# Performance work log

Hardware: AMD Instinct MI355X
Metric: run time of the kernel (lower is better)

The kernel has to match this reference:

```python
import jax, jax.numpy as jnp
import numpy as np

N_NODES = 50000
N_EDGES = 800000
NODE = 128
EDGE = 16
H = 96
OUT = 64
L = 3
BN_EPS = 1e-5


def setup_inputs() -> dict:
    key = jax.random.key(0)
    ks = iter(jax.random.split(key, 48))
    def rn(shape, s=0.05):
        return jax.random.normal(next(ks), shape, dtype=jnp.float32) * s
    inp = {
        "x": jax.random.normal(next(ks), (N_NODES, NODE), dtype=jnp.float32),
        "edge_index": jax.random.randint(next(ks), (2, N_EDGES), 0, N_NODES, dtype=jnp.int32),
        "edge_attr": jax.random.normal(next(ks), (N_EDGES, EDGE), dtype=jnp.float32),
        # GCNConv (layer 0)
        "gcn_lin_w": rn((NODE, H)), "gcn_lin_b": rn((H,)),
        "gcn_root": rn((1, H)),
        "gcn_bw1": rn((EDGE, H)), "gcn_bb1": rn((H,)),
        "gcn_bw2": rn((H, H)), "gcn_bb2": rn((H,)),
        # GINConv layers 1..L-1 (stacked)
        "gin_bw1": rn((L - 1, EDGE, H)), "gin_bb1": rn((L - 1, H)),
        "gin_bw2": rn((L - 1, H, H)), "gin_bb2": rn((L - 1, H)),
        "gin_mw1": rn((L - 1, H, H)), "gin_mb1": rn((L - 1, H)),
        "gin_mw2": rn((L - 1, H, H)), "gin_mb2": rn((L - 1, H)),
        "gin_eps": jnp.zeros((L - 1,), jnp.float32),
        # BatchNorm (eval mode, running stats)
        "bn_gamma": jnp.ones((L, H), jnp.float32),
        "bn_beta": jnp.zeros((L, H), jnp.float32),
        "bn_mean": rn((L, H)),
        "bn_var": jnp.ones((L, H), jnp.float32) + jax.random.uniform(next(ks), (L, H), dtype=jnp.float32) * 0.1,
        # head
        "fc1_w": rn((L * H, H)), "fc1_b": rn((H,)),
        "fc2_w": rn((H, OUT)), "fc2_b": rn((OUT,)),
    }
    return inp


def _bn(x, gamma, beta, mean, var):
    return (x - mean) * jax.lax.rsqrt(var + BN_EPS) * gamma + beta


def reference(x, edge_index, edge_attr,
              gcn_lin_w, gcn_lin_b, gcn_root, gcn_bw1, gcn_bb1, gcn_bw2, gcn_bb2,
              gin_bw1, gin_bb1, gin_bw2, gin_bb2, gin_mw1, gin_mb1, gin_mw2, gin_mb2, gin_eps,
              bn_gamma, bn_beta, bn_mean, bn_var,
              fc1_w, fc1_b, fc2_w, fc2_b):
    n = x.shape[0]
    row, col = edge_index[0], edge_index[1]  # source, target

    # ---- Layer 0: GCNConv with edge attributes ----
    h = x @ gcn_lin_w + gcn_lin_b                                    # [N,H]
    ee = jax.nn.relu(edge_attr @ gcn_bw1 + gcn_bb1) @ gcn_bw2 + gcn_bb2  # [E,H]
    deg = jax.ops.segment_sum(jnp.ones_like(row, dtype=h.dtype), row, num_segments=n) + 1.0
    dinv = jax.lax.rsqrt(deg)                                        # deg >= 1, no inf
    norm = dinv[row] * dinv[col]                                     # [E]
    msg = norm[:, None] * jax.nn.relu(h[row] + ee)                   # [E,H]
    agg = jax.ops.segment_sum(msg, col, num_segments=n)              # [N,H]
    h = agg + jax.nn.relu(h + gcn_root) / deg[:, None]
    h = _bn(jax.nn.relu(h), bn_gamma[0], bn_beta[0], bn_mean[0], bn_var[0])
    feats = [h]

    # ---- Layers 1..L-1: GINConv with edge attributes ----
    for i in range(L - 1):
        ee = jax.nn.relu(edge_attr @ gin_bw1[i] + gin_bb1[i]) @ gin_bw2[i] + gin_bb2[i]  # [E,H]
        agg = jax.ops.segment_sum(jax.nn.relu(h[row] + ee), col, num_segments=n)          # [N,H]
        z = (1.0 + gin_eps[i]) * h + agg
        z = jax.nn.relu(z @ gin_mw1[i] + gin_mb1[i]) @ gin_mw2[i] + gin_mb2[i]
        h = _bn(jax.nn.relu(z), bn_gamma[i + 1], bn_beta[i + 1], bn_mean[i + 1], bn_var[i + 1])
        feats.append(h)

    cat = jnp.concatenate(feats, axis=-1)                            # [N, L*H]
    y = jax.nn.relu(cat @ fc1_w + fc1_b)                             # dropout is eval-mode identity
    return y @ fc2_w + fc2_b                                         # [N, OUT]
```

## Files before the change

### kernel.cpp

```cpp
#include <hip/hip_runtime.h>
#include <hip/hip_bf16.h>


#define HH 96
#define EDGEF 16
#define CAT (3 * HH)

typedef __attribute__((ext_vector_type(8))) short bf16x8;
typedef __attribute__((ext_vector_type(4))) float f32x4;
typedef __attribute__((ext_vector_type(4))) unsigned short ubf16x4;
typedef __attribute__((ext_vector_type(2))) unsigned uint2v;

typedef union { bf16x8 v; unsigned u[4]; } bfpack8;
typedef union { ubf16x4 v; unsigned u[2]; } bfpack4;

__device__ __forceinline__ unsigned short f2bf(float f) {
    unsigned u = __float_as_uint(f);
    u += 0x7fffu + ((u >> 16) & 1u);
    return (unsigned short)(u >> 16);
}
__device__ __forceinline__ float bf2f(unsigned short s) {
    return __uint_as_float(((unsigned)s) << 16);
}
__device__ __forceinline__ unsigned pkbf2(float lo, float hi) {
    __hip_bfloat162 b = __float22bfloat162_rn(make_float2(lo, hi));
    union { __hip_bfloat162 b2; unsigned u; } cv; cv.b2 = b; return cv.u;
}

template <int K, int F, int AMODE, int EPI>
__global__ __launch_bounds__(256) void node_gemm(
    const void* __restrict__ Aptr, int lda,
    const float* __restrict__ agg,
    const float* __restrict__ eps_arr, int li,
    const float* __restrict__ W, const float* __restrict__ bias,
    void* __restrict__ Cptr, int ldc,
    unsigned short* __restrict__ bf_copy,
    const float* __restrict__ gamma, const float* __restrict__ beta,
    const float* __restrict__ mean, const float* __restrict__ var,
    int M)
{
    constexpr int SW = ((K * 2) % 128 == 0) ? 7 : 3;
    constexpr int NFT = F / 16;
    __shared__ __align__(16) short s_wt[F * K];

    const int tid = threadIdx.x;
    const int lane = tid & 63;
    const int w = tid >> 6;
    const int lr = lane & 15;
    const int lg = lane >> 4;

    for (int idx = tid; idx < F * K; idx += 256) {
        int f = idx / K, k = idx - f * K;
        s_wt[idx ^ ((f & SW) << 3)] = (short)f2bf(W[k * F + f]);
    }
    __syncthreads();

    const int R0 = blockIdx.x * 64 + 16 * w;
    const int Ra = min(R0 + lr, M - 1);

    float e1 = 0.f;
    if (AMODE == 2) e1 = 1.f + eps_arr[li];

    f32x4 acc[NFT];
#pragma unroll
    for (int ft = 0; ft < NFT; ++ft) {
        float b = bias[16 * ft + lr];
        acc[ft][0] = b; acc[ft][1] = b; acc[ft][2] = b; acc[ft][3] = b;
    }

#pragma unroll
    for (int kt = 0; kt < K / 32; ++kt) {
        bf16x8 ae;
        if (AMODE == 0) {
            const float* ap = (const float*)Aptr + (size_t)Ra * lda + 32 * kt + 8 * lg;
            f32x4 a0 = *(const f32x4*)ap;
            f32x4 a1 = *(const f32x4*)(ap + 4);
            bfpack8 p;
            p.u[0] = pkbf2(a0[0], a0[1]); p.u[1] = pkbf2(a0[2], a0[3]);
            p.u[2] = pkbf2(a1[0], a1[1]); p.u[3] = pkbf2(a1[2], a1[3]);
            ae = p.v;
        } else if (AMODE == 1) {
            ae = *(const bf16x8*)((const unsigned short*)Aptr + (size_t)Ra * lda + 32 * kt + 8 * lg);
        } else {
            const unsigned short* hp = (const unsigned short*)Aptr + (size_t)Ra * lda + 32 * kt + 8 * lg;
            bf16x8 h8 = *(const bf16x8*)hp;
            const float* gp = agg + (size_t)Ra * HH + 32 * kt + 8 * lg;
            f32x4 g0 = *(const f32x4*)gp;
            f32x4 g1 = *(const f32x4*)(gp + 4);
            float t0 = fmaf(e1, bf2f((unsigned short)h8[0]), g0[0]);
            float t1 = fmaf(e1, bf2f((unsigned short)h8[1]), g0[1]);
            float t2 = fmaf(e1, bf2f((unsigned short)h8[2]), g0[2]);
            float t3 = fmaf(e1, bf2f((unsigned short)h8[3]), g0[3]);
            float t4 = fmaf(e1, bf2f((unsigned short)h8[4]), g1[0]);
            float t5 = fmaf(e1, bf2f((unsigned short)h8[5]), g1[1]);
            float t6 = fmaf(e1, bf2f((unsigned short)h8[6]), g1[2]);
            float t7 = fmaf(e1, bf2f((unsigned short)h8[7]), g1[3]);
            bfpack8 p;
            p.u[0] = pkbf2(t0, t1); p.u[1] = pkbf2(t2, t3);
            p.u[2] = pkbf2(t4, t5); p.u[3] = pkbf2(t6, t7);
            ae = p.v;
        }
#pragma unroll
        for (int ft = 0; ft < NFT; ++ft) {
            bf16x8 bw = *(const bf16x8*)&s_wt[((lr + 16 * ft) * K + 32 * kt + 8 * lg) ^ ((lr & SW) << 3)];
            acc[ft] = __builtin_amdgcn_mfma_f32_16x16x32_bf16(ae, bw, acc[ft], 0, 0, 0);
        }
    }

    float scale[NFT], shiftv[NFT];
    if (EPI == 2) {
#pragma unroll
        for (int ft = 0; ft < NFT; ++ft) {
            int col = 16 * ft + lr;
            float s = gamma[col] * rsqrtf(var[col] + 1e-5f);
            scale[ft] = s;
            shiftv[ft] = beta[col] - mean[col] * s;
        }
    }
#pragma unroll
    for (int reg = 0; reg < 4; ++reg) {
        int r = R0 + 4 * lg + reg;
        if (r < M) {
#pragma unroll
            for (int ft = 0; ft < NFT; ++ft) {
                int col = 16 * ft + lr;
                float v = acc[ft][reg];
                if (EPI == 0) {
                    ((float*)Cptr)[(size_t)r * ldc + col] = v;
                } else if (EPI == 1) {
                    ((unsigned short*)Cptr)[(size_t)r * ldc + col] = f2bf(fmaxf(v, 0.f));
                } else if (EPI == 2) {
                    float z = fmaxf(v, 0.f) * scale[ft] + shiftv[ft];
                    unsigned short zb = f2bf(z);
                    ((unsigned short*)Cptr)[(size_t)r * ldc + col] = zb;
                    bf_copy[(size_t)r * F + col] = zb;
                } else {
                    ((float*)Cptr)[(size_t)r * ldc + col] = v;
                    bf_copy[(size_t)r * F + col] = f2bf(v);
                }
            }
        }
    }
}

__global__ void init_kernel(float* __restrict__ deg, int* __restrict__ cnt, int N)
{
    int i = blockIdx.x * blockDim.x + threadIdx.x;
    if (i < N) { deg[i] = 1.f; cnt[i] = 0; }
}

__global__ void count_kernel(const int* __restrict__ row, const int* __restrict__ col,
                             float* __restrict__ deg, int* __restrict__ cnt, int E)
{
    int e = blockIdx.x * blockDim.x + threadIdx.x;
    if (e < E) {
        atomicAdd(&deg[row[e]], 1.f);
        atomicAdd(&cnt[col[e]], 1);
    }
}

__global__ void scan1_kernel(const int* __restrict__ cnt, int* __restrict__ start,
                             int* __restrict__ bsum, int N)
{
    __shared__ int s[256];
    int tid = threadIdx.x;
    int i = blockIdx.x * 256 + tid;
    int v = (i < N) ? cnt[i] : 0;
    s[tid] = v;
    __syncthreads();
#pragma unroll
    for (int off = 1; off < 256; off <<= 1) {
        int t = (tid >= off) ? s[tid - off] : 0;
        __syncthreads();
        s[tid] += t;
        __syncthreads();
    }
    if (i < N) start[i] = s[tid] - v;
    if (tid == 255) bsum[blockIdx.x] = s[255];
}

__global__ void scan2_kernel(int* __restrict__ bsum, int nb)
{
    __shared__ int s[256];
    int tid = threadIdx.x;
    int v = (tid < nb) ? bsum[tid] : 0;
    s[tid] = v;
    __syncthreads();
#pragma unroll
    for (int off = 1; off < 256; off <<= 1) {
        int t = (tid >= off) ? s[tid - off] : 0;
        __syncthreads();
        s[tid] += t;
        __syncthreads();
    }
    if (tid < nb) bsum[tid] = s[tid] - v;
}

__global__ void scan3_kernel(int* __restrict__ start, const int* __restrict__ bsum,
                             int* __restrict__ cursor,
                             const float* __restrict__ deg, float* __restrict__ dinv,
                             int N, int E)
{
    int i = blockIdx.x * blockDim.x + threadIdx.x;
    if (i < N) {
        int f = start[i] + bsum[i >> 8];
        start[i] = f;
        cursor[i] = f;
        dinv[i] = rsqrtf(deg[i]);
    } else if (i == N) {
        start[N] = E;
    }
}

__global__ void scatter_ea_kernel(const int* __restrict__ row, const int* __restrict__ col,
                                  int* __restrict__ cursor,
                                  const float* __restrict__ ea,
                                  int* __restrict__ row_sorted,
                                  unsigned short* __restrict__ eas, int E)
{
    int e = blockIdx.x * blockDim.x + threadIdx.x;
    if (e >= E) return;
    int c = col[e];
    int p = atomicAdd(&cursor[c], 1);
    row_sorted[p] = row[e];
    const float* src = ea + (size_t)e * EDGEF;
    f32x4 v0 = *(const f32x4*)(src);
    f32x4 v1 = *(const f32x4*)(src + 4);
    f32x4 v2 = *(const f32x4*)(src + 8);
    f32x4 v3 = *(const f32x4*)(src + 12);
    bfpack8 o0, o1;
    o0.u[0] = pkbf2(v0[0], v0[1]); o0.u[1] = pkbf2(v0[2], v0[3]);
    o0.u[2] = pkbf2(v1[0], v1[1]); o0.u[3] = pkbf2(v1[2], v1[3]);
    o1.u[0] = pkbf2(v2[0], v2[1]); o1.u[1] = pkbf2(v2[2], v2[3]);
    o1.u[2] = pkbf2(v3[0], v3[1]); o1.u[3] = pkbf2(v3[2], v3[3]);
    *(bf16x8*)(eas + (size_t)p * EDGEF) = o0.v;
    *(bf16x8*)(eas + (size_t)p * EDGEF + 8) = o1.v;
}

template <bool GCN>
__global__ __launch_bounds__(256, 4) void edge_kernel(
    const unsigned short* __restrict__ ea_sorted,
    const int* __restrict__ row_sorted,
    const int* __restrict__ seg_start,
    const float* __restrict__ bw1, const float* __restrict__ bb1,
    const float* __restrict__ bw2, const float* __restrict__ bb2,
    const unsigned short* __restrict__ hbf,
    const float* __restrict__ dinv,
    float* __restrict__ agg,
    int N)
{
    __shared__ __align__(16) short s_bw2T[96][104];
    __shared__ __align__(16) short s_bw1T[96][16];
    __shared__ __align__(16) short s_t[4][16][104];
    __shared__ float s_bias[192];

    const int tid = threadIdx.x;
    const int lane = tid & 63;
    const int w = tid >> 6;
    const int lr = lane & 15;
    const int lg = lane >> 4;

    for (int idx = tid; idx < HH * HH; idx += 256) {
        int k = idx / HH, f = idx - k * HH;
        s_bw2T[f][k] = (short)f2bf(bw2[idx]);
    }
    for (int idx = tid; idx < EDGEF * HH; idx += 256) {
        int k = idx / HH, f = idx - k * HH;
        s_bw1T[f][k] = (short)f2bf(bw1[idx]);
    }
    if (tid < HH) { s_bias[tid] = bb1[tid]; s_bias[HH + tid] = bb2[tid]; }
    __syncthreads();

    bf16x8 bwf[6];
#pragma unroll
    for (int ft = 0; ft < 6; ++ft) {
        bf16x8 z;
#pragma unroll
        for (int j = 0; j < 8; ++j) z[j] = 0;
        if (lg < 2) z = *(const bf16x8*)&s_bw1T[lr + 16 * ft][8 * lg];
        bwf[ft] = z;
    }

    const int nwaves = gridDim.x * 4;

    for (int c = blockIdx.x * 4 + w; c < N; c += nwaves) {
        const int s0 = seg_start[c];
        const int s1 = seg_start[c + 1];
        const float dinv_c = GCN ? dinv[c] : 1.f;

        f32x4 acc[6];
#pragma unroll
        for (int ft = 0; ft < 6; ++ft) { acc[ft][0]=0.f; acc[ft][1]=0.f; acc[ft][2]=0.f; acc[ft][3]=0.f; }

        for (int b = s0; b < s1; b += 16) {
            const int epos = b + lr;
            const bool vld = (epos < s1);
            const int epc = vld ? epos : s0;
            const int r = row_sorted[epc];

            const unsigned short* hrow = hbf + (size_t)r * HH + 24 * lg;
            bf16x8 h0 = *(const bf16x8*)(hrow);
            bf16x8 h1 = *(const bf16x8*)(hrow + 8);
            bf16x8 h2 = *(const bf16x8*)(hrow + 16);

            const float msk = vld ? (GCN ? dinv[r] * dinv_c : 1.f) : 0.f;

            bf16x8 ae = *(const bf16x8*)(ea_sorted + (size_t)epc * EDGEF + 8 * (lg & 1));

#pragma unroll
            for (int ft = 0; ft < 6; ++ft) {
                f32x4 ci = *(const f32x4*)&s_bias[16 * ft + 4 * lg];
                f32x4 t4 = __builtin_amdgcn_mfma_f32_16x16x32_bf16(bwf[ft], ae, ci, 0, 0, 0);
                float v0 = fmaxf(t4[0], 0.f);
                float v1 = fmaxf(t4[1], 0.f);
                float v2 = fmaxf(t4[2], 0.f);
                float v3 = fmaxf(t4[3], 0.f);
                uint2v uu;
                uu[0] = pkbf2(v0, v1);
                uu[1] = pkbf2(v2, v3);
                *(uint2v*)&s_t[w][lr][16 * ft + 4 * lg] = uu;
            }
            __builtin_amdgcn_wave_barrier();

            bf16x8 bt[3];
#pragma unroll
            for (int kt = 0; kt < 3; ++kt)
                bt[kt] = *(const bf16x8*)&s_t[w][lr][8 * lg + 32 * kt];
            __builtin_amdgcn_wave_barrier();

            *(bf16x8*)&s_t[w][lr][24 * lg]      = h0;
            *(bf16x8*)&s_t[w][lr][24 * lg + 8]  = h1;
            *(bf16x8*)&s_t[w][lr][24 * lg + 16] = h2;
            __builtin_amdgcn_wave_barrier();

#pragma unroll
            for (int ft = 0; ft < 6; ++ft) {
                const int fb = 16 * ft + 4 * lg;
                f32x4 ee = *(const f32x4*)&s_bias[HH + fb];
#pragma unroll
                for (int kt = 0; kt < 3; ++kt) {
                    bf16x8 aw = *(const bf16x8*)&s_bw2T[lr + 16 * ft][8 * lg + 32 * kt];
                    ee = __builtin_amdgcn_mfma_f32_16x16x32_bf16(aw, bt[kt], ee, 0, 0, 0);
                }
                ubf16x4 hv = *(const ubf16x4*)&s_t[w][lr][fb];
#pragma unroll
                for (int reg = 0; reg < 4; ++reg) {
                    float m = fmaxf(bf2f(hv[reg]) + ee[reg], 0.f);
                    acc[ft][reg] = fmaf(m, msk, acc[ft][reg]);
                }
            }
        }

#pragma unroll
        for (int ft = 0; ft < 6; ++ft) {
#pragma unroll
            for (int reg = 0; reg < 4; ++reg) {
                float v = acc[ft][reg];
                v += __shfl_xor(v, 1);
                v += __shfl_xor(v, 2);
                v += __shfl_xor(v, 4);
                v += __shfl_xor(v, 8);
                acc[ft][reg] = v;
            }
        }
        if (lr == 0) {
#pragma unroll
            for (int ft = 0; ft < 6; ++ft)
                *(f32x4*)&agg[(size_t)c * HH + 16 * ft + 4 * lg] = acc[ft];
        }
    }
}

__global__ void gcn_epilogue_kernel(
    const float* __restrict__ agg, const float* __restrict__ hbuf,
    const float* __restrict__ root, const float* __restrict__ deg,
    const float* __restrict__ gamma, const float* __restrict__ beta,
    const float* __restrict__ mean, const float* __restrict__ var,
    unsigned short* __restrict__ featsbf, unsigned short* __restrict__ hb, int N)
{
    int idx = blockIdx.x * blockDim.x + threadIdx.x;
    if (idx >= N * (HH / 4)) return;
    int n = idx / (HH / 4), q = idx - n * (HH / 4);
    int f0 = 4 * q;
    f32x4 a  = *(const f32x4*)&agg[(size_t)n * HH + f0];
    f32x4 h  = *(const f32x4*)&hbuf[(size_t)n * HH + f0];
    f32x4 rt = *(const f32x4*)&root[f0];
    f32x4 gm = *(const f32x4*)&gamma[f0];
    f32x4 bt = *(const f32x4*)&beta[f0];
    f32x4 mn = *(const f32x4*)&mean[f0];
    f32x4 vr = *(const f32x4*)&var[f0];
    float di = 1.f / deg[n];
    float vv[4];
#pragma unroll
    for (int j = 0; j < 4; ++j) {
        float self = fmaxf(h[j] + rt[j], 0.f) * di;
        float v = fmaxf(a[j] + self, 0.f);
        vv[j] = (v - mn[j]) * rsqrtf(vr[j] + 1e-5f) * gm[j] + bt[j];
    }
    bfpack4 o;
    o.u[0] = pkbf2(vv[0], vv[1]);
    o.u[1] = pkbf2(vv[2], vv[3]);
    *(ubf16x4*)&featsbf[(size_t)n * CAT + f0] = o.v;
    *(ubf16x4*)&hb[(size_t)n * HH + f0] = o.v;
}

extern "C" void kernel_launch(void* const* d_in, const int* in_sizes, int n_in,
                              void* d_out, int out_size, void* d_ws, size_t ws_size,
                              hipStream_t stream)
{
    const float* x         = (const float*)d_in[0];
    const int*   eidx      = (const int*)d_in[1];
    const float* edge_attr = (const float*)d_in[2];
    const float* gcn_lin_w = (const float*)d_in[3];
    const float* gcn_lin_b = (const float*)d_in[4];
    const float* gcn_root  = (const float*)d_in[5];
    const float* gcn_bw1   = (const float*)d_in[6];
    const float* gcn_bb1   = (const float*)d_in[7];
    const float* gcn_bw2   = (const float*)d_in[8];
    const float* gcn_bb2   = (const float*)d_in[9];
    const float* gin_bw1   = (const float*)d_in[10];
    const float* gin_bb1   = (const float*)d_in[11];
    const float* gin_bw2   = (const float*)d_in[12];
    const float* gin_bb2   = (const float*)d_in[13];
    const float* gin_mw1   = (const float*)d_in[14];
    const float* gin_mb1   = (const float*)d_in[15];
    const float* gin_mw2   = (const float*)d_in[16];
    const float* gin_mb2   = (const float*)d_in[17];
    const float* gin_eps   = (const float*)d_in[18];
    const float* bn_gamma  = (const float*)d_in[19];
    const float* bn_beta   = (const float*)d_in[20];
    const float* bn_mean   = (const float*)d_in[21];
    const float* bn_var    = (const float*)d_in[22];
    const float* fc1_w     = (const float*)d_in[23];
    const float* fc1_b     = (const float*)d_in[24];
    const float* fc2_w     = (const float*)d_in[25];
    const float* fc2_b     = (const float*)d_in[26];
    float* out = (float*)d_out;

    const int N = in_sizes[0] / 128;
    const int E = in_sizes[1] / 2;
    const int* row = eidx;
    const int* col = eidx + E;

    char* ws = (char*)d_ws;
    float* deg        = (float*)(ws);
    float* dinv       = (float*)(ws + (size_t)256 * 1024);
    int*   seg_start  = (int*)(ws + (size_t)512 * 1024);
    int*   cursor     = (int*)(ws + (size_t)768 * 1024);
    int*   bsum       = (int*)(ws + (size_t)1024 * 1024);
    int*   row_sorted = (int*)(ws + (size_t)1088 * 1024);
    unsigned short* ea_sorted = (unsigned short*)(ws + (size_t)8 * 1024 * 1024);
    unsigned short* hb        = (unsigned short*)(ws + (size_t)34 * 1024 * 1024);
    float* hbuf   = (float*)(ws + (size_t)44 * 1024 * 1024);
    float* agg    = (float*)(ws + (size_t)64 * 1024 * 1024);
    unsigned short* featsbf = (unsigned short*)(ws + (size_t)84 * 1024 * 1024);
    unsigned short* z1bf    = (unsigned short*)(ws + (size_t)113 * 1024 * 1024);
    unsigned short* r1bf    = (unsigned short*)(ws + (size_t)123 * 1024 * 1024);

    const int ew_blocks = 1024;
    const int q_grid = (N * (HH / 4) + 255) / 256;
    const int gemm_grid = (N + 63) / 64;
    const int e_grid = (E + 255) / 256;
    const int n_grid = (N + 255) / 256;
    const int nchunks = (N + 255) / 256;

    init_kernel<<<n_grid, 256, 0, stream>>>(deg, cursor, N);
    count_kernel<<<e_grid, 256, 0, stream>>>(row, col, deg, cursor, E);
    scan1_kernel<<<nchunks, 256, 0, stream>>>(cursor, seg_start, bsum, N);
    scan2_kernel<<<1, 256, 0, stream>>>(bsum, nchunks);
    scan3_kernel<<<(N + 256) / 256, 256, 0, stream>>>(seg_start, bsum, cursor, deg, dinv, N, E);
    scatter_ea_kernel<<<e_grid, 256, 0, stream>>>(row, col, cursor, edge_attr,
                                                  row_sorted, ea_sorted, E);

    node_gemm<128, 96, 0, 3><<<gemm_grid, 256, 0, stream>>>(
        x, 128, nullptr, nullptr, 0, gcn_lin_w, gcn_lin_b,
        hbuf, HH, hb, nullptr, nullptr, nullptr, nullptr, N);
    edge_kernel<true><<<ew_blocks, 256, 0, stream>>>(
        ea_sorted, row_sorted, seg_start,
        gcn_bw1, gcn_bb1, gcn_bw2, gcn_bb2, hb, dinv, agg, N);
    gcn_epilogue_kernel<<<q_grid, 256, 0, stream>>>(
        agg, hbuf, gcn_root, deg, bn_gamma, bn_beta, bn_mean, bn_var, featsbf, hb, N);

    for (int i = 0; i < 2; ++i) {
        edge_kernel<false><<<ew_blocks, 256, 0, stream>>>(
            ea_sorted, row_sorted, seg_start,
            gin_bw1 + (size_t)i * EDGEF * HH, gin_bb1 + i * HH,
            gin_bw2 + (size_t)i * HH * HH, gin_bb2 + i * HH,
            hb, dinv, agg, N);
        node_gemm<96, 96, 2, 1><<<gemm_grid, 256, 0, stream>>>(
            hb, HH, agg, gin_eps, i,
            gin_mw1 + (size_t)i * HH * HH, gin_mb1 + i * HH,
            z1bf, HH, nullptr, nullptr, nullptr, nullptr, nullptr, N);
        node_gemm<96, 96, 1, 2><<<gemm_grid, 256, 0, stream>>>(
            z1bf, HH, nullptr, nullptr, 0,
            gin_mw2 + (size_t)i * HH * HH, gin_mb2 + i * HH,
            featsbf + (i + 1) * HH, CAT, hb,
            bn_gamma + (i + 1) * HH, bn_beta + (i + 1) * HH,
            bn_mean + (i + 1) * HH, bn_var + (i + 1) * HH, N);
    }

    node_gemm<288, 96, 1, 1><<<gemm_grid, 256, 0, stream>>>(
        featsbf, CAT, nullptr, nullptr, 0, fc1_w, fc1_b,
        r1bf, HH, nullptr, nullptr, nullptr, nullptr, nullptr, N);
    node_gemm<96, 64, 1, 0><<<gemm_grid, 256, 0, stream>>>(
        r1bf, HH, nullptr, nullptr, 0, fc2_w, fc2_b,
        out, 64, nullptr, nullptr, nullptr, nullptr, nullptr, N);
}
```

Baseline: 676.1 us.

## Fuse GIN MLP GEMMs into one kernel and load h directly in edge kernel

```diff
diff --git a/kernel.cpp b/kernel.cpp
--- a/kernel.cpp
+++ b/kernel.cpp
@@ -30,13 +30,9 @@
 template <int K, int F, int AMODE, int EPI>
 __global__ __launch_bounds__(256) void node_gemm(
     const void* __restrict__ Aptr, int lda,
-    const float* __restrict__ agg,
-    const float* __restrict__ eps_arr, int li,
     const float* __restrict__ W, const float* __restrict__ bias,
     void* __restrict__ Cptr, int ldc,
     unsigned short* __restrict__ bf_copy,
-    const float* __restrict__ gamma, const float* __restrict__ beta,
-    const float* __restrict__ mean, const float* __restrict__ var,
     int M)
 {
     constexpr int SW = ((K * 2) % 128 == 0) ? 7 : 3;
@@ -57,9 +53,6 @@
 
     const int R0 = blockIdx.x * 64 + 16 * w;
     const int Ra = min(R0 + lr, M - 1);
-
-    float e1 = 0.f;
-    if (AMODE == 2) e1 = 1.f + eps_arr[li];
 
     f32x4 acc[NFT];
 #pragma unroll
@@ -79,26 +72,8 @@
             p.u[0] = pkbf2(a0[0], a0[1]); p.u[1] = pkbf2(a0[2], a0[3]);
             p.u[2] = pkbf2(a1[0], a1[1]); p.u[3] = pkbf2(a1[2], a1[3]);
             ae = p.v;
-        } else if (AMODE == 1) {
+        } else {
             ae = *(const bf16x8*)((const unsigned short*)Aptr + (size_t)Ra * lda + 32 * kt + 8 * lg);
-        } else {
-            const unsigned short* hp = (const unsigned short*)Aptr + (size_t)Ra * lda + 32 * kt + 8 * lg;
-            bf16x8 h8 = *(const bf16x8*)hp;
-            const float* gp = agg + (size_t)Ra * HH + 32 * kt + 8 * lg;
-            f32x4 g0 = *(const f32x4*)gp;
-            f32x4 g1 = *(const f32x4*)(gp + 4);
-            float t0 = fmaf(e1, bf2f((unsigned short)h8[0]), g0[0]);
-            float t1 = fmaf(e1, bf2f((unsigned short)h8[1]), g0[1]);
-            float t2 = fmaf(e1, bf2f((unsigned short)h8[2]), g0[2]);
-            float t3 = fmaf(e1, bf2f((unsigned short)h8[3]), g0[3]);
-            float t4 = fmaf(e1, bf2f((unsigned short)h8[4]), g1[0]);
-            float t5 = fmaf(e1, bf2f((unsigned short)h8[5]), g1[1]);
-            float t6 = fmaf(e1, bf2f((unsigned short)h8[6]), g1[2]);
-            float t7 = fmaf(e1, bf2f((unsigned short)h8[7]), g1[3]);
-            bfpack8 p;
-            p.u[0] = pkbf2(t0, t1); p.u[1] = pkbf2(t2, t3);
-            p.u[2] = pkbf2(t4, t5); p.u[3] = pkbf2(t6, t7);
-            ae = p.v;
         }
 #pragma unroll
         for (int ft = 0; ft < NFT; ++ft) {
@@ -107,16 +82,6 @@
         }
     }
 
-    float scale[NFT], shiftv[NFT];
-    if (EPI == 2) {
-#pragma unroll
-        for (int ft = 0; ft < NFT; ++ft) {
-            int col = 16 * ft + lr;
-            float s = gamma[col] * rsqrtf(var[col] + 1e-5f);
-            scale[ft] = s;
-            shiftv[ft] = beta[col] - mean[col] * s;
-        }
-    }
 #pragma unroll
     for (int reg = 0; reg < 4; ++reg) {
         int r = R0 + 4 * lg + reg;
@@ -129,15 +94,123 @@
                     ((float*)Cptr)[(size_t)r * ldc + col] = v;
                 } else if (EPI == 1) {
                     ((unsigned short*)Cptr)[(size_t)r * ldc + col] = f2bf(fmaxf(v, 0.f));
-                } else if (EPI == 2) {
-                    float z = fmaxf(v, 0.f) * scale[ft] + shiftv[ft];
-                    unsigned short zb = f2bf(z);
-                    ((unsigned short*)Cptr)[(size_t)r * ldc + col] = zb;
-                    bf_copy[(size_t)r * F + col] = zb;
                 } else {
                     ((float*)Cptr)[(size_t)r * ldc + col] = v;
                     bf_copy[(size_t)r * F + col] = f2bf(v);
                 }
+            }
+        }
+    }
+}
+
+__global__ __launch_bounds__(256) void gin_mlp(
+    const unsigned short* __restrict__ hb_in,
+    const float* __restrict__ agg,
+    const float* __restrict__ eps_arr, int li,
+    const float* __restrict__ mw1, const float* __restrict__ mb1,
+    const float* __restrict__ mw2, const float* __restrict__ mb2,
+    const float* __restrict__ gamma, const float* __restrict__ beta,
+    const float* __restrict__ mean, const float* __restrict__ var,
+    unsigned short* __restrict__ featsbf, int slot,
+    unsigned short* __restrict__ hb_out,
+    int M)
+{
+    __shared__ __align__(16) short s_w1t[96][104];
+    __shared__ __align__(16) short s_w2t[96][104];
+    __shared__ __align__(16) short s_z[4][16][104];
+    __shared__ float s_b[192];
+
+    const int tid = threadIdx.x;
+    const int lane = tid & 63;
+    const int w = tid >> 6;
+    const int lr = lane & 15;
+    const int lg = lane >> 4;
+
+    for (int idx = tid; idx < HH * HH; idx += 256) {
+        int k = idx / HH, f = idx - k * HH;
+        s_w1t[f][k] = (short)f2bf(mw1[idx]);
+        s_w2t[f][k] = (short)f2bf(mw2[idx]);
+    }
+    if (tid < HH) { s_b[tid] = mb1[tid]; s_b[HH + tid] = mb2[tid]; }
+    __syncthreads();
+
+    const int R0 = blockIdx.x * 64 + 16 * w;
+    const int Ra = min(R0 + lr, M - 1);
+    const float e1 = 1.f + eps_arr[li];
+
+    bf16x8 inf[3];
+#pragma unroll
+    for (int kt = 0; kt < 3; ++kt) {
+        const unsigned short* hp = hb_in + (size_t)Ra * HH + 32 * kt + 8 * lg;
+        bf16x8 h8 = *(const bf16x8*)hp;
+        const float* gp = agg + (size_t)Ra * HH + 32 * kt + 8 * lg;
+        f32x4 g0 = *(const f32x4*)gp;
+        f32x4 g1 = *(const f32x4*)(gp + 4);
+        float t0 = fmaf(e1, bf2f((unsigned short)h8[0]), g0[0]);
+        float t1 = fmaf(e1, bf2f((unsigned short)h8[1]), g0[1]);
+        float t2 = fmaf(e1, bf2f((unsigned short)h8[2]), g0[2]);
+        float t3 = fmaf(e1, bf2f((unsigned short)h8[3]), g0[3]);
+        float t4 = fmaf(e1, bf2f((unsigned short)h8[4]), g1[0]);
+        float t5 = fmaf(e1, bf2f((unsigned short)h8[5]), g1[1]);
+        float t6 = fmaf(e1, bf2f((unsigned short)h8[6]), g1[2]);
+        float t7 = fmaf(e1, bf2f((unsigned short)h8[7]), g1[3]);
+        bfpack8 p;
+        p.u[0] = pkbf2(t0, t1); p.u[1] = pkbf2(t2, t3);
+        p.u[2] = pkbf2(t4, t5); p.u[3] = pkbf2(t6, t7);
+        inf[kt] = p.v;
+    }
+
+#pragma unroll
+    for (int ft = 0; ft < 6; ++ft) {
+        f32x4 t4v = *(const f32x4*)&s_b[16 * ft + 4 * lg];
+#pragma unroll
+        for (int kt = 0; kt < 3; ++kt) {
+            bf16x8 aw = *(const bf16x8*)&s_w1t[16 * ft + lr][32 * kt + 8 * lg];
+            t4v = __builtin_amdgcn_mfma_f32_16x16x32_bf16(aw, inf[kt], t4v, 0, 0, 0);
+        }
+        uint2v uu;
+        uu[0] = pkbf2(fmaxf(t4v[0], 0.f), fmaxf(t4v[1], 0.f));
+        uu[1] = pkbf2(fmaxf(t4v[2], 0.f), fmaxf(t4v[3], 0.f));
+        *(uint2v*)&s_z[w][lr][16 * ft + 4 * lg] = uu;
+    }
+    __builtin_amdgcn_wave_barrier();
+
+    bf16x8 az[3];
+#pragma unroll
+    for (int kt = 0; kt < 3; ++kt)
+        az[kt] = *(const bf16x8*)&s_z[w][lr][32 * kt + 8 * lg];
+
+    f32x4 acc[6];
+#pragma unroll
+    for (int ft = 0; ft < 6; ++ft) {
+        float b = s_b[HH + 16 * ft + lr];
+        acc[ft][0] = b; acc[ft][1] = b; acc[ft][2] = b; acc[ft][3] = b;
+#pragma unroll
+        for (int kt = 0; kt < 3; ++kt) {
+            bf16x8 bw = *(const bf16x8*)&s_w2t[16 * ft + lr][32 * kt + 8 * lg];
+            acc[ft] = __builtin_amdgcn_mfma_f32_16x16x32_bf16(az[kt], bw, acc[ft], 0, 0, 0);
+        }
+    }
+
+    float scale[6], shiftv[6];
+#pragma unroll
+    for (int ft = 0; ft < 6; ++ft) {
+        int col = 16 * ft + lr;
+        float s = gamma[col] * rsqrtf(var[col] + 1e-5f);
+        scale[ft] = s;
+        shiftv[ft] = beta[col] - mean[col] * s;
+    }
+#pragma unroll
+    for (int reg = 0; reg < 4; ++reg) {
+        int r = R0 + 4 * lg + reg;
+        if (r < M) {
+#pragma unroll
+            for (int ft = 0; ft < 6; ++ft) {
+                int col = 16 * ft + lr;
+                float z = fmaxf(acc[ft][reg], 0.f) * scale[ft] + shiftv[ft];
+                unsigned short zb = f2bf(z);
+                featsbf[(size_t)r * CAT + slot * HH + col] = zb;
+                hb_out[(size_t)r * HH + col] = zb;
             }
         }
     }
@@ -298,10 +371,11 @@
             const int epc = vld ? epos : s0;
             const int r = row_sorted[epc];
 
-            const unsigned short* hrow = hbf + (size_t)r * HH + 24 * lg;
-            bf16x8 h0 = *(const bf16x8*)(hrow);
-            bf16x8 h1 = *(const bf16x8*)(hrow + 8);
-            bf16x8 h2 = *(const bf16x8*)(hrow + 16);
+            const unsigned short* hrow = hbf + (size_t)r * HH + 4 * lg;
+            ubf16x4 hv[6];
+#pragma unroll
+            for (int ft = 0; ft < 6; ++ft)
+                hv[ft] = *(const ubf16x4*)(hrow + 16 * ft);
 
             const float msk = vld ? (GCN ? dinv[r] * dinv_c : 1.f) : 0.f;
 
@@ -311,13 +385,9 @@
             for (int ft = 0; ft < 6; ++ft) {
                 f32x4 ci = *(const f32x4*)&s_bias[16 * ft + 4 * lg];
                 f32x4 t4 = __builtin_amdgcn_mfma_f32_16x16x32_bf16(bwf[ft], ae, ci, 0, 0, 0);
-                float v0 = fmaxf(t4[0], 0.f);
-                float v1 = fmaxf(t4[1], 0.f);
-                float v2 = fmaxf(t4[2], 0.f);
-                float v3 = fmaxf(t4[3], 0.f);
                 uint2v uu;
-                uu[0] = pkbf2(v0, v1);
-                uu[1] = pkbf2(v2, v3);
+                uu[0] = pkbf2(fmaxf(t4[0], 0.f), fmaxf(t4[1], 0.f));
+                uu[1] = pkbf2(fmaxf(t4[2], 0.f), fmaxf(t4[3], 0.f));
                 *(uint2v*)&s_t[w][lr][16 * ft + 4 * lg] = uu;
             }
             __builtin_amdgcn_wave_barrier();
@@ -326,12 +396,6 @@
 #pragma unroll
             for (int kt = 0; kt < 3; ++kt)
                 bt[kt] = *(const bf16x8*)&s_t[w][lr][8 * lg + 32 * kt];
-            __builtin_amdgcn_wave_barrier();
-
-            *(bf16x8*)&s_t[w][lr][24 * lg]      = h0;
-            *(bf16x8*)&s_t[w][lr][24 * lg + 8]  = h1;
-            *(bf16x8*)&s_t[w][lr][24 * lg + 16] = h2;
-            __builtin_amdgcn_wave_barrier();
 
 #pragma unroll
             for (int ft = 0; ft < 6; ++ft) {
@@ -342,10 +406,9 @@
                     bf16x8 aw = *(const bf16x8*)&s_bw2T[lr + 16 * ft][8 * lg + 32 * kt];
                     ee = __builtin_amdgcn_mfma_f32_16x16x32_bf16(aw, bt[kt], ee, 0, 0, 0);
                 }
-                ubf16x4 hv = *(const ubf16x4*)&s_t[w][lr][fb];
 #pragma unroll
                 for (int reg = 0; reg < 4; ++reg) {
-                    float m = fmaxf(bf2f(hv[reg]) + ee[reg], 0.f);
+                    float m = fmaxf(bf2f(hv[ft][reg]) + ee[reg], 0.f);
                     acc[ft][reg] = fmaf(m, msk, acc[ft][reg]);
                 }
             }
@@ -454,7 +517,6 @@
     float* hbuf   = (float*)(ws + (size_t)44 * 1024 * 1024);
     float* agg    = (float*)(ws + (size_t)64 * 1024 * 1024);
     unsigned short* featsbf = (unsigned short*)(ws + (size_t)84 * 1024 * 1024);
-    unsigned short* z1bf    = (unsigned short*)(ws + (size_t)113 * 1024 * 1024);
     unsigned short* r1bf    = (unsigned short*)(ws + (size_t)123 * 1024 * 1024);
 
     const int ew_blocks = 1024;
@@ -473,8 +535,7 @@
                                                   row_sorted, ea_sorted, E);
 
     node_gemm<128, 96, 0, 3><<<gemm_grid, 256, 0, stream>>>(
-        x, 128, nullptr, nullptr, 0, gcn_lin_w, gcn_lin_b,
-        hbuf, HH, hb, nullptr, nullptr, nullptr, nullptr, N);
+        x, 128, gcn_lin_w, gcn_lin_b, hbuf, HH, hb, N);
     edge_kernel<true><<<ew_blocks, 256, 0, stream>>>(
         ea_sorted, row_sorted, seg_start,
         gcn_bw1, gcn_bb1, gcn_bw2, gcn_bb2, hb, dinv, agg, N);
@@ -487,22 +548,17 @@
             gin_bw1 + (size_t)i * EDGEF * HH, gin_bb1 + i * HH,
             gin_bw2 + (size_t)i * HH * HH, gin_bb2 + i * HH,
             hb, dinv, agg, N);
-        node_gemm<96, 96, 2, 1><<<gemm_grid, 256, 0, stream>>>(
-            hb, HH, agg, gin_eps, i,
+        gin_mlp<<<gemm_grid, 256, 0, stream>>>(
+            hb, agg, gin_eps, i,
             gin_mw1 + (size_t)i * HH * HH, gin_mb1 + i * HH,
-            z1bf, HH, nullptr, nullptr, nullptr, nullptr, nullptr, N);
-        node_gemm<96, 96, 1, 2><<<gemm_grid, 256, 0, stream>>>(
-            z1bf, HH, nullptr, nullptr, 0,
             gin_mw2 + (size_t)i * HH * HH, gin_mb2 + i * HH,
-            featsbf + (i + 1) * HH, CAT, hb,
             bn_gamma + (i + 1) * HH, bn_beta + (i + 1) * HH,
-            bn_mean + (i + 1) * HH, bn_var + (i + 1) * HH, N);
+            bn_mean + (i + 1) * HH, bn_var + (i + 1) * HH,
+            featsbf, i + 1, hb, N);
     }
 
     node_gemm<288, 96, 1, 1><<<gemm_grid, 256, 0, stream>>>(
-        featsbf, CAT, nullptr, nullptr, 0, fc1_w, fc1_b,
-        r1bf, HH, nullptr, nullptr, nullptr, nullptr, nullptr, N);
+        featsbf, CAT, fc1_w, fc1_b, r1bf, HH, nullptr, N);
     node_gemm<96, 64, 1, 0><<<gemm_grid, 256, 0, stream>>>(
-        r1bf, HH, nullptr, nullptr, 0, fc2_w, fc2_b,
-        out, 64, nullptr, nullptr, nullptr, nullptr, nullptr, N);
-}
+        r1bf, HH, fc2_w, fc2_b, out, 64, nullptr, N);
+}
```

Measured after the change: 597.4 us (median of 2 runs). 11.6% less time.
